# Optimization experiments

Measured on AMD Instinct MI355X. Metric: run time of the kernel, lower is better.

Reference implementation:

```python
import jax, jax.numpy as jnp
import numpy as np

EPS = 1e-8
LAMBDA_SOFTMAX = 9.0   # opt.lambda_softmax (SCAN t2i default)
ITERATION_STEP = 2     # opt.iteration_step
LEAKY_SLOPE = 0.1      # clipped_l2norm leaky relu slope


def l2norm(x, axis):
    norm = jnp.sqrt(jnp.sum(x * x, axis=axis, keepdims=True)) + EPS
    return x / norm


def cosine_sim(a, b, axis):
    w12 = jnp.sum(a * b, axis=axis)
    w1 = jnp.linalg.norm(a, axis=axis)
    w2 = jnp.linalg.norm(b, axis=axis)
    return w12 / jnp.clip(w1 * w2, EPS)


def func_attention_t2i(query, context):
    """query: [C, I, T, D] caption words per (caption, image) pair;
    context: [I, R, D] image regions. Returns weightedContext [C, I, T, D]."""
    # attn = bmm(context, query^T) -> [C, I, R, T]
    attn = jnp.einsum('ird,citd->cirt', context, query)
    # raw_feature_norm == 'clipped_l2norm': LeakyReLU(0.1) then l2norm over queryL
    attn = jax.nn.leaky_relu(attn, LEAKY_SLOPE)
    attn = l2norm(attn, axis=-1)
    # transpose -> [C, I, T, R]; temperature softmax over sourceL (regions)
    attn = jnp.swapaxes(attn, -1, -2)
    attn = jax.nn.softmax(attn * LAMBDA_SOFTMAX, axis=-1)
    # weightedContext = bmm(context^T, attn^T)^T -> [C, I, T, D]
    return jnp.einsum('citr,ird->citd', attn, context)


def setup_inputs() -> dict:
    key = jax.random.key(0)
    ks = jax.random.split(key, 4)
    B, R, T, D = 32, 36, 40, 1024
    # encoder outputs are l2-normalized along the feature dim
    img_emb = l2norm(jax.random.normal(ks[0], (B, R, D), jnp.float32), axis=-1)
    cap_emb = l2norm(jax.random.normal(ks[1], (B, T, D), jnp.float32), axis=-1)
    W_lin = jax.random.normal(ks[2], (2 * D, D), jnp.float32) * 0.02
    b_lin = jnp.zeros((D,), jnp.float32)
    W_gate = jax.random.normal(ks[3], (2 * D, D), jnp.float32) * 0.02
    b_gate = jnp.zeros((D,), jnp.float32)
    return dict(img_emb=img_emb, cap_emb=cap_emb,
                W_lin=W_lin, b_lin=b_lin, W_gate=W_gate, b_gate=b_gate)


def reference(img_emb, cap_emb, W_lin, b_lin, W_gate, b_gate):
    """xattn_score_Text_IMRAM (t2i) with gated memory, summed over iterations.
    Returns similarity score matrix [n_image, n_caption]."""
    C, T, D = cap_emb.shape
    I = img_emb.shape[0]
    # cap_i_expand: each caption repeated across all images
    cap_exp = jnp.broadcast_to(cap_emb[:, None], (C, I, T, D))
    query = cap_exp
    score = jnp.zeros((I, C), cap_emb.dtype)
    for _ in range(ITERATION_STEP):
        wc = func_attention_t2i(query, img_emb)            # [C, I, T, D]
        # cosine similarity per word vs original caption words, mean over words
        row_sim = cosine_sim(cap_exp, wc, axis=-1).mean(-1)  # [C, I]
        score = score + row_sim.T                           # [I, C]
        # gated_memory_t2i
        cat = jnp.concatenate([query, wc], axis=-1)         # [C, I, T, 2D]
        upd = jnp.tanh(cat @ W_lin + b_lin)
        gate = jax.nn.sigmoid(cat @ W_gate + b_gate)
        query = query * gate + upd * (1.0 - gate)
    return score
```

## Files before the change

kernel.cpp:

```cpp
#include <hip/hip_runtime.h>
#include <stdint.h>


typedef unsigned short u16;
typedef __attribute__((ext_vector_type(8))) short bf16x8;
typedef __attribute__((ext_vector_type(4))) float f32x4;

#define MFMA_BF16(a, b, c) __builtin_amdgcn_mfma_f32_16x16x32_bf16((a), (b), (c), 0, 0, 0)

__device__ __forceinline__ float bf2f(u16 u) {
  union { unsigned v; float f; } x; x.v = ((unsigned)u) << 16; return x.f;
}
__device__ __forceinline__ u16 f2bf(float f) {
  union { float f; unsigned v; } x; x.f = f;
  return (u16)((x.v + 0x7fffu + ((x.v >> 16) & 1u)) >> 16);
}
__device__ __forceinline__ float frcp(float x) { return __builtin_amdgcn_rcpf(x); }
__device__ __forceinline__ void gl2lds16(const u16* g, u16* l) {
  __builtin_amdgcn_global_load_lds((const __attribute__((address_space(1))) void*)g,
                                   (__attribute__((address_space(3))) void*)l, 16, 0, 0);
}

__global__ void prep_k(const float* __restrict__ img, const float* __restrict__ cap,
                       const float* __restrict__ Wl, const float* __restrict__ Wg,
                       u16* __restrict__ imgb, u16* __restrict__ capb,
                       u16* __restrict__ WTl, u16* __restrict__ WTg,
                       float* __restrict__ cnorm, u16* __restrict__ cwF0) {
  __shared__ u16 tile[32][33];
  const int b = blockIdx.x, tid = threadIdx.x;
  if (b < 2432) {
    const float* src; u16* dst; int idx;
    if (b < 1152) { src = img; dst = imgb; idx = (b * 256 + tid) * 4; }
    else { src = cap; dst = capb; idx = ((b - 1152) * 256 + tid) * 4; }
    const float4 v = *(const float4*)(src + idx);
    u16 o[4] = {f2bf(v.x), f2bf(v.y), f2bf(v.z), f2bf(v.w)};
    *(uint2*)(dst + idx) = *(const uint2*)o;
  } else if (b < 6528) {
    const int b2 = b - 2432;
    const int bx = b2 & 63, by = (b2 >> 6) & 31, bz = b2 >> 11;
    const float* src = bz ? Wg : Wl;
    u16* dst = bz ? WTg : WTl;
    const int k0 = bx * 32, n0 = by * 32;
    const int tx = tid & 31, ty = tid >> 5;
#pragma unroll
    for (int j = 0; j < 4; ++j)
      tile[ty + 8 * j][tx] = f2bf(src[(size_t)(k0 + ty + 8 * j) * 1024 + n0 + tx]);
    __syncthreads();
#pragma unroll
    for (int j = 0; j < 4; ++j)
      dst[(size_t)(n0 + ty + 8 * j) * 2048 + k0 + tx] = tile[tx][ty + 8 * j];
  } else if (b < 6848) {
    const int wv = tid >> 6, lane = tid & 63;
    const int row = (b - 6528) * 4 + wv;
    const float* p = cap + ((size_t)row << 10) + lane * 16;
    float s = 0.f;
#pragma unroll
    for (int e = 0; e < 16; ++e) { float v = p[e]; s += v * v; }
#pragma unroll
    for (int off = 32; off > 0; off >>= 1) s += __shfl_down(s, off, 64);
    if (lane == 0) cnorm[row] = sqrtf(s);
  } else {
    const int idx = ((b - 6848) * 256 + tid) * 8;
    uint4 z; z.x = z.y = z.z = z.w = 0u;
    *(uint4*)(cwF0 + idx) = z;
  }
}

__global__ __launch_bounds__(256, 2) void gemms_k(
    const u16* __restrict__ capb, const u16* __restrict__ imgb,
    const u16* __restrict__ WTl, const u16* __restrict__ WTg,
    u16* __restrict__ preL, u16* __restrict__ preG,
    u16* __restrict__ cwFL, u16* __restrict__ cwFG,
    const float* __restrict__ bL, const float* __restrict__ bG,
    float* __restrict__ S1, u16* __restrict__ Ghi, u16* __restrict__ Glo) {
  __shared__ __align__(16) char lsU[20480];
  const int bid = blockIdx.x;
  const int tid = threadIdx.x;
  const int wv = tid >> 6, lane = tid & 63;
  const int quad = lane >> 4, l15 = lane & 15;
  const bf16x8 zero8 = {0, 0, 0, 0, 0, 0, 0, 0};

  if (bid < 640) {
    u16* lsA = (u16*)lsU;
    u16* lsB = (u16*)(lsU + 4096);
    const int i = bid & 31, m0 = (bid >> 5) * 64;
    const u16* B = imgb + (size_t)i * 36 * 1024;
    f32x4 acc[3];
#pragma unroll
    for (int b = 0; b < 3; ++b) acc[b] = (f32x4){0.f, 0.f, 0.f, 0.f};
    for (int kt = 0; kt < 32; ++kt) {
      if (kt) __syncthreads();
      const int rr = tid >> 2, j = tid & 3;
      const int js = j ^ ((rr >> 2) & 3);
      gl2lds16(capb + (size_t)(m0 + rr) * 1024 + kt * 32 + js * 8,
               lsA + (size_t)(wv * 64) * 8);
      const int rc = rr < 36 ? rr : 35;
      gl2lds16(B + (size_t)rc * 1024 + kt * 32 + js * 8,
               lsB + (size_t)(wv * 64) * 8);
      __syncthreads();
      const int ra = wv * 16 + l15;
      const bf16x8 a2 = *(const bf16x8*)(lsA + ra * 32 + (quad ^ ((ra >> 2) & 3)) * 8);
      bf16x8 b3[3];
#pragma unroll
      for (int nf = 0; nf < 3; ++nf) {
        const int rb = nf * 16 + l15;
        const bf16x8 bv = *(const bf16x8*)(lsB + rb * 32 + (quad ^ ((rb >> 2) & 3)) * 8);
        b3[nf] = (rb < 36) ? bv : zero8;
      }
#pragma unroll
      for (int nf = 0; nf < 3; ++nf) acc[nf] = MFMA_BF16(a2, b3[nf], acc[nf]);
    }
#pragma unroll
    for (int nf = 0; nf < 3; ++nf)
#pragma unroll
      for (int rg = 0; rg < 4; ++rg) {
        const int m = m0 + wv * 16 + quad * 4 + rg;
        S1[((size_t)i * 1280 + m) * 48 + nf * 16 + l15] = acc[nf][rg];
      }
  } else if (bid < 944) {
    u16* lsA = (u16*)lsU;
    u16* lsBl = (u16*)(lsU + 4096);
    u16* lsBg = (u16*)(lsU + 12288);
    const int b2 = bid - 640;
    const int bm = b2 >> 3, bn = b2 & 7;
    const bool iscap = bm < 20;
    const u16* A = iscap ? capb + (size_t)bm * 64 * 1024
                         : imgb + (size_t)(bm - 20) * 64 * 1024;
    const int kofs = iscap ? 0 : 1024;
    const int wm = (wv & 1) * 32, wn = (wv >> 1) * 64;
    f32x4 accL[2][4], accG[2][4];
#pragma unroll
    for (int a = 0; a < 2; ++a)
#pragma unroll
      for (int b = 0; b < 4; ++b) {
        accL[a][b] = (f32x4){0.f, 0.f, 0.f, 0.f};
        accG[a][b] = (f32x4){0.f, 0.f, 0.f, 0.f};
      }
    for (int kt = 0; kt < 32; ++kt) {
      if (kt) __syncthreads();
      {
        const int row = tid >> 2, c8 = tid & 3;
        const int js = c8 ^ (row & 3);
        gl2lds16(A + (size_t)row * 1024 + kt * 32 + js * 8,
                 lsA + (size_t)(wv * 64) * 8);
      }
#pragma unroll
      for (int s = 0; s < 2; ++s) {
        const int idx = s * 256 + tid;
        const int row = idx >> 2, c8 = idx & 3;
        const int js = c8 ^ (row & 3);
        const size_t bro = (size_t)(bn * 128 + row) * 2048 + kofs + kt * 32 + js * 8;
        gl2lds16(WTl + bro, lsBl + (size_t)(s * 256 + wv * 64) * 8);
        gl2lds16(WTg + bro, lsBg + (size_t)(s * 256 + wv * 64) * 8);
      }
      __syncthreads();
      bf16x8 af[2], bl8[4], bg8[4];
#pragma unroll
      for (int mt = 0; mt < 2; ++mt) {
        const int ra = wm + mt * 16 + l15;
        af[mt] = *(const bf16x8*)(lsA + ra * 32 + (quad ^ (ra & 3)) * 8);
      }
#pragma unroll
      for (int nt = 0; nt < 4; ++nt) {
        const int rb = wn + nt * 16 + l15;
        const int off = rb * 32 + (quad ^ (rb & 3)) * 8;
        bl8[nt] = *(const bf16x8*)(lsBl + off);
        bg8[nt] = *(const bf16x8*)(lsBg + off);
      }
#pragma unroll
      for (int mt = 0; mt < 2; ++mt)
#pragma unroll
        for (int nt = 0; nt < 4; ++nt) {
          accL[mt][nt] = MFMA_BF16(af[mt], bl8[nt], accL[mt][nt]);
          accG[mt][nt] = MFMA_BF16(af[mt], bg8[nt], accG[mt][nt]);
        }
    }
#pragma unroll
    for (int mt = 0; mt < 2; ++mt)
#pragma unroll
      for (int nt = 0; nt < 4; ++nt) {
        const int n = bn * 128 + wn + nt * 16 + l15;
        if (iscap) {
          const float blv = bL[n], bgv = bG[n];
#pragma unroll
          for (int r = 0; r < 4; ++r) {
            const int m = bm * 64 + wm + mt * 16 + quad * 4 + r;
            preL[((size_t)m << 10) + n] = f2bf(accL[mt][nt][r] + blv);
            preG[((size_t)m << 10) + n] = f2bf(accG[mt][nt][r] + bgv);
          }
        } else {
          const int db = n >> 4, l15d = n & 15;
#pragma unroll
          for (int r = 0; r < 4; ++r) {
            const int mi = (bm - 20) * 64 + wm + mt * 16 + quad * 4 + r;
            const int i = (mi * 3641) >> 17;
            const int r36 = mi - i * 36;
            const int ksr = r36 >> 5, qd = (r36 & 31) >> 3, e = r36 & 7;
            const size_t gb =
                ((((size_t)i * 64 + db) * 2 + ksr) * 64 + qd * 16 + l15d) * 8 + e;
            cwFL[gb] = f2bf(accL[mt][nt][r]);
            cwFG[gb] = f2bf(accG[mt][nt][r]);
          }
        }
      }
  } else {
    float* lsS = (float*)lsU;
    const int i = bid - 944;
    for (int k = tid; k < 48 * 52; k += 256) lsS[k] = 0.f;
    const u16* arow[3]; bool avalid[3];
#pragma unroll
    for (int mt = 0; mt < 3; ++mt) {
      const int r = mt * 16 + l15;
      avalid[mt] = r < 36;
      arow[mt] = imgb + ((size_t)(i * 36 + (r < 36 ? r : 35)) << 10);
    }
    f32x4 acc[3][3];
#pragma unroll
    for (int a = 0; a < 3; ++a)
#pragma unroll
      for (int b = 0; b < 3; ++b) acc[a][b] = (f32x4){0.f, 0.f, 0.f, 0.f};
    for (int kk = wv * 8; kk < wv * 8 + 8; ++kk) {
      const int ko = kk * 32 + quad * 8;
      bf16x8 af[3];
#pragma unroll
      for (int mt = 0; mt < 3; ++mt)
        af[mt] = avalid[mt] ? *(const bf16x8*)(arow[mt] + ko) : zero8;
#pragma unroll
      for (int mt = 0; mt < 3; ++mt)
#pragma unroll
        for (int nt = 0; nt < 3; ++nt)
          acc[mt][nt] = MFMA_BF16(af[mt], af[nt], acc[mt][nt]);
    }
    __syncthreads();
#pragma unroll
    for (int mt = 0; mt < 3; ++mt)
#pragma unroll
      for (int nt = 0; nt < 3; ++nt)
#pragma unroll
        for (int rg = 0; rg < 4; ++rg)
          atomicAdd(&lsS[(nt * 16 + l15) * 52 + mt * 16 + quad * 4 + rg],
                    acc[mt][nt][rg]);
    __syncthreads();
    if (wv == 0) {
#pragma unroll
      for (int nt = 0; nt < 3; ++nt) {
        const int rp = nt * 16 + l15;
#pragma unroll
        for (int mt = 0; mt < 3; ++mt) {
          const f32x4 g = *(const f32x4*)&lsS[rp * 52 + mt * 16 + quad * 4];
          u16 hv[4], lv[4];
#pragma unroll
          for (int rg = 0; rg < 4; ++rg) {
            hv[rg] = f2bf(g[rg]);
            lv[rg] = f2bf(g[rg] - bf2f(hv[rg]));
          }
          const size_t gb = ((size_t)i * 48 + rp) * 64 + mt * 16 + quad * 4;
          *(uint2*)(Ghi + gb) = *(const uint2*)hv;
          *(uint2*)(Glo + gb) = *(const uint2*)lv;
        }
      }
    }
    for (int k = tid; k < 48 * 16; k += 256) {
      const size_t gb = ((size_t)i * 48 + (k >> 4)) * 64 + 48 + (k & 15);
      Ghi[gb] = 0; Glo[gb] = 0;
    }
  }
}

__global__ __launch_bounds__(256, 4) void gates2_k(
    const u16* __restrict__ cwFL, const u16* __restrict__ cwFG,
    const u16* __restrict__ P1, const u16* __restrict__ preL,
    const u16* __restrict__ preG, const u16* __restrict__ capb,
    const u16* __restrict__ imgb, float* __restrict__ S2) {
  __shared__ __align__(16) u16 lsPre[3][32 * 128];
  __shared__ __align__(16) float lsS2f[32 * 52];
  const int tid = threadIdx.x;
  const int bid = blockIdx.x;
  const int i = bid & 31, ctt = bid >> 5;
  const int ct0 = ctt * 32;
  const int wv = tid >> 6, lane = tid & 63;
  const int quad = lane >> 4, l15 = lane & 15;

  for (int k = tid; k < 32 * 52; k += 256) lsS2f[k] = 0.f;

  bf16x8 bp[2][2];
#pragma unroll
  for (int nt = 0; nt < 2; ++nt)
#pragma unroll
    for (int ks = 0; ks < 2; ++ks)
      bp[nt][ks] = *(const bf16x8*)(
          P1 + ((size_t)i * 1280 + ct0 + nt * 16 + l15) * 64 + ks * 32 + quad * 8);

  const u16* arow[3]; bool avalid[3];
#pragma unroll
  for (int mt = 0; mt < 3; ++mt) {
    const int r = mt * 16 + l15;
    avalid[mt] = r < 36;
    arow[mt] = imgb + ((size_t)(i * 36 + (r < 36 ? r : 35)) << 10);
  }
  const bf16x8 zero8 = {0, 0, 0, 0, 0, 0, 0, 0};

  f32x4 acc2[3][2];
#pragma unroll
  for (int a = 0; a < 3; ++a)
#pragma unroll
    for (int b = 0; b < 2; ++b) acc2[a][b] = (f32x4){0.f, 0.f, 0.f, 0.f};

#define STAGE(dcx)                                                          \
  {                                                                         \
    _Pragma("unroll")                                                       \
    for (int s = 0; s < 2; ++s) {                                           \
      const int idx = s * 256 + tid;                                        \
      const int rr = idx >> 4, j = idx & 15;                                \
      const int js = j ^ (rr & 7);                                          \
      const size_t src = (size_t)(ct0 + rr) * 1024 + (dcx) * 128 + js * 8;  \
      const size_t dst = (size_t)(s * 256 + wv * 64) * 8;                   \
      gl2lds16(preL + src, lsPre[0] + dst);                                 \
      gl2lds16(preG + src, lsPre[1] + dst);                                 \
      gl2lds16(capb + src, lsPre[2] + dst);                                 \
    }                                                                       \
  }

  STAGE(0);
  for (int dc = 0; dc < 8; ++dc) {
    __syncthreads();

    f32x4 accL[2][2], accG[2][2];
#pragma unroll
    for (int a = 0; a < 2; ++a)
#pragma unroll
      for (int b = 0; b < 2; ++b) {
        accL[a][b] = (f32x4){0.f, 0.f, 0.f, 0.f};
        accG[a][b] = (f32x4){0.f, 0.f, 0.f, 0.f};
      }
#pragma unroll
    for (int mt = 0; mt < 2; ++mt)
#pragma unroll
      for (int ks = 0; ks < 2; ++ks) {
        const int db = dc * 8 + wv * 2 + mt;
        const size_t co = ((((size_t)i * 64 + db) * 2 + ks) * 64 + lane) * 8;
        const bf16x8 al = *(const bf16x8*)(cwFL + co);
        const bf16x8 ag = *(const bf16x8*)(cwFG + co);
#pragma unroll
        for (int nt = 0; nt < 2; ++nt) {
          accL[mt][nt] = MFMA_BF16(al, bp[nt][ks], accL[mt][nt]);
          accG[mt][nt] = MFMA_BF16(ag, bp[nt][ks], accG[mt][nt]);
        }
      }

    uint2 ovv[2][2];
#pragma unroll
    for (int mt = 0; mt < 2; ++mt) {
      const int drel = wv * 32 + mt * 16 + quad * 4;
      const int j = drel >> 3;
#pragma unroll
      for (int nt = 0; nt < 2; ++nt) {
        const int rr = nt * 16 + l15;
        const int off = rr * 128 + (j ^ (rr & 7)) * 8 + (quad & 1) * 4;
        const uint2 plv = *(const uint2*)(lsPre[0] + off);
        const uint2 pgv = *(const uint2*)(lsPre[1] + off);
        const uint2 cfv = *(const uint2*)(lsPre[2] + off);
        const float pl4[4] = {bf2f((u16)(plv.x & 0xffffu)), bf2f((u16)(plv.x >> 16)),
                              bf2f((u16)(plv.y & 0xffffu)), bf2f((u16)(plv.y >> 16))};
        const float pg4[4] = {bf2f((u16)(pgv.x & 0xffffu)), bf2f((u16)(pgv.x >> 16)),
                              bf2f((u16)(pgv.y & 0xffffu)), bf2f((u16)(pgv.y >> 16))};
        const float cf4[4] = {bf2f((u16)(cfv.x & 0xffffu)), bf2f((u16)(cfv.x >> 16)),
                              bf2f((u16)(cfv.y & 0xffffu)), bf2f((u16)(cfv.y >> 16))};
        u16 ov[4];
#pragma unroll
        for (int rg = 0; rg < 4; ++rg) {
          const float aL = accL[mt][nt][rg] + pl4[rg];
          const float aG = accG[mt][nt][rg] + pg4[rg];
          const float g = frcp(1.f + __expf(-aG));
          const float u = 2.f * frcp(1.f + __expf(-2.f * aL)) - 1.f;
          ov[rg] = f2bf(cf4[rg] * g + u * (1.f - g));
        }
        ovv[mt][nt] = *(const uint2*)ov;
      }
    }
    __syncthreads();
    if (dc < 7) STAGE(dc + 1);

#pragma unroll
    for (int nt = 0; nt < 2; ++nt) {
      unsigned w[4];
#pragma unroll
      for (int j2 = 0; j2 < 4; ++j2) {
        const int srcl = ((quad & 1) * 2 + (j2 >> 1)) * 16 + l15;
        const unsigned a0 =
            __shfl((j2 & 1) ? ovv[0][nt].y : ovv[0][nt].x, srcl, 64);
        const unsigned a1 =
            __shfl((j2 & 1) ? ovv[1][nt].y : ovv[1][nt].x, srcl, 64);
        w[j2] = (quad >= 2) ? a1 : a0;
      }
      union { unsigned u[4]; bf16x8 v; } bq;
      bq.u[0] = w[0]; bq.u[1] = w[1]; bq.u[2] = w[2]; bq.u[3] = w[3];
      const int dg = dc * 128 + wv * 32 + quad * 8;
#pragma unroll
      for (int mt = 0; mt < 3; ++mt) {
        const bf16x8 af = avalid[mt] ? *(const bf16x8*)(arow[mt] + dg) : zero8;
        acc2[mt][nt] = MFMA_BF16(af, bq.v, acc2[mt][nt]);
      }
    }
  }
#undef STAGE
#pragma unroll
  for (int mt = 0; mt < 3; ++mt)
#pragma unroll
    for (int nt = 0; nt < 2; ++nt)
#pragma unroll
      for (int rg = 0; rg < 4; ++rg)
        atomicAdd(&lsS2f[(nt * 16 + l15) * 52 + mt * 16 + quad * 4 + rg],
                  acc2[mt][nt][rg]);
  __syncthreads();
  for (int idx = tid; idx < 384; idx += 256) {
    const int ct = idx / 12, rq = idx % 12;
    *(f32x4*)(S2 + ((size_t)i * 1280 + ct0 + ct) * 48 + rq * 4) =
        *(const f32x4*)&lsS2f[ct * 52 + rq * 4];
  }
}

template <int PASS2>
__global__ __launch_bounds__(256, 2) void score_k(
    const float* __restrict__ Ssm, const float* __restrict__ S1,
    const u16* __restrict__ Ghi, const u16* __restrict__ Glo,
    const float* __restrict__ cnorm, u16* __restrict__ P1,
    float* __restrict__ sim1, float* __restrict__ score) {
  __shared__ __align__(16) u16 lsP[4][48 * 72];
  const int tid = threadIdx.x;
  const int wv = tid >> 6, lane = tid & 63;
  const int quad = lane >> 4, l15 = lane & 15;
  const int pair = blockIdx.x * 4 + wv;
  const int c = pair >> 5, i = pair & 31;
  u16* lsPw = lsP[wv];
  for (int k = lane; k < 1728; k += 64) ((unsigned*)lsPw)[k] = 0u;

  float sS[3][3][4], s1f[3][3][4];
  const float* Sb = Ssm + ((size_t)i * 1280 + c * 40) * 48;
  const float* S1b = S1 + ((size_t)i * 1280 + c * 40) * 48;
#pragma unroll
  for (int nt = 0; nt < 3; ++nt) {
    const int t = nt * 16 + l15;
    const int tr = t < 40 ? t : 39;
#pragma unroll
    for (int mt = 0; mt < 3; ++mt) {
      f32x4 v = *(const f32x4*)(Sb + (size_t)tr * 48 + mt * 16 + quad * 4);
      if (t >= 40) v = (f32x4){0.f, 0.f, 0.f, 0.f};
#pragma unroll
      for (int rg = 0; rg < 4; ++rg) sS[mt][nt][rg] = v[rg];
      if (PASS2) {
        const f32x4 w = *(const f32x4*)(S1b + (size_t)tr * 48 + mt * 16 + quad * 4);
#pragma unroll
        for (int rg = 0; rg < 4; ++rg) s1f[mt][nt][rg] = w[rg];
      } else {
#pragma unroll
        for (int rg = 0; rg < 4; ++rg) s1f[mt][nt][rg] = v[rg];
      }
    }
  }

  float rn[3][4];
#pragma unroll
  for (int mt = 0; mt < 3; ++mt)
#pragma unroll
    for (int rg = 0; rg < 4; ++rg) {
      float s2 = 0.f;
#pragma unroll
      for (int nt = 0; nt < 3; ++nt) {
        float v = sS[mt][nt][rg]; v = v > 0.f ? v : 0.1f * v; s2 += v * v;
      }
      s2 += __shfl_xor(s2, 1, 64); s2 += __shfl_xor(s2, 2, 64);
      s2 += __shfl_xor(s2, 4, 64); s2 += __shfl_xor(s2, 8, 64);
      rn[mt][rg] = sqrtf(s2) + 1e-8f;
    }
  float mx[3] = {-3.0e38f, -3.0e38f, -3.0e38f};
#pragma unroll
  for (int mt = 0; mt < 3; ++mt)
#pragma unroll
    for (int nt = 0; nt < 3; ++nt)
#pragma unroll
      for (int rg = 0; rg < 4; ++rg) {
        const int r = mt * 16 + quad * 4 + rg;
        float v = sS[mt][nt][rg]; v = v > 0.f ? v : 0.1f * v;
        float zz = 9.f * v / rn[mt][rg];
        zz = (r < 36) ? zz : -3.0e38f;
        sS[mt][nt][rg] = zz;
        mx[nt] = fmaxf(mx[nt], zz);
      }
#pragma unroll
  for (int nt = 0; nt < 3; ++nt) {
    mx[nt] = fmaxf(mx[nt], __shfl_xor(mx[nt], 16, 64));
    mx[nt] = fmaxf(mx[nt], __shfl_xor(mx[nt], 32, 64));
  }
  float ss[3] = {0.f, 0.f, 0.f};
#pragma unroll
  for (int mt = 0; mt < 3; ++mt)
#pragma unroll
    for (int nt = 0; nt < 3; ++nt)
#pragma unroll
      for (int rg = 0; rg < 4; ++rg) {
        const float e = __expf(sS[mt][nt][rg] - mx[nt]);
        sS[mt][nt][rg] = e; ss[nt] += e;
      }
#pragma unroll
  for (int nt = 0; nt < 3; ++nt) {
    ss[nt] += __shfl_xor(ss[nt], 16, 64);
    ss[nt] += __shfl_xor(ss[nt], 32, 64);
    ss[nt] = 1.f / ss[nt];
  }
#pragma unroll
  for (int nt = 0; nt < 3; ++nt) {
    const int t = nt * 16 + l15;
#pragma unroll
    for (int mt = 0; mt < 3; ++mt) {
#pragma unroll
      for (int rg = 0; rg < 4; ++rg) sS[mt][nt][rg] *= ss[nt];
      if (t < 40) {
        u16 pv[4];
#pragma unroll
        for (int rg = 0; rg < 4; ++rg) pv[rg] = f2bf(sS[mt][nt][rg]);
        *(uint2*)(lsPw + t * 72 + mt * 16 + quad * 4) = *(const uint2*)pv;
      }
    }
  }

  float pnv[3] = {0.f, 0.f, 0.f};
#pragma unroll
  for (int nt = 0; nt < 3; ++nt)
#pragma unroll
    for (int mt = 0; mt < 3; ++mt)
#pragma unroll
      for (int rg = 0; rg < 4; ++rg) pnv[nt] += sS[mt][nt][rg] * s1f[mt][nt][rg];

  if (!PASS2) {
    for (int idx = lane; idx < 320; idx += 64) {
      const int t = idx >> 3, j = idx & 7;
      *(uint4*)(P1 + ((size_t)i * 1280 + c * 40 + t) * 64 + j * 8) =
          *(const uint4*)(lsPw + t * 72 + j * 8);
    }
  }

  bf16x8 afA[3][2];
#pragma unroll
  for (int mtT = 0; mtT < 3; ++mtT)
#pragma unroll
    for (int ks = 0; ks < 2; ++ks)
      afA[mtT][ks] =
          *(const bf16x8*)(lsPw + (mtT * 16 + l15) * 72 + ks * 32 + quad * 8);
  f32x4 gp[3][3];
#pragma unroll
  for (int a = 0; a < 3; ++a)
#pragma unroll
    for (int b = 0; b < 3; ++b) gp[a][b] = (f32x4){0.f, 0.f, 0.f, 0.f};
#pragma unroll
  for (int ks = 0; ks < 2; ++ks)
#pragma unroll
    for (int mtG = 0; mtG < 3; ++mtG) {
      const size_t gb = ((size_t)i * 48 + mtG * 16 + l15) * 64 + ks * 32 + quad * 8;
      const bf16x8 gh = *(const bf16x8*)(Ghi + gb);
      const bf16x8 gl = *(const bf16x8*)(Glo + gb);
#pragma unroll
      for (int mtT = 0; mtT < 3; ++mtT) {
        gp[mtG][mtT] = MFMA_BF16(gh, afA[mtT][ks], gp[mtG][mtT]);
        gp[mtG][mtT] = MFMA_BF16(gl, afA[mtT][ks], gp[mtG][mtT]);
      }
    }
  float pwv[3] = {0.f, 0.f, 0.f};
#pragma unroll
  for (int nt = 0; nt < 3; ++nt)
#pragma unroll
    for (int mt = 0; mt < 3; ++mt)
#pragma unroll
      for (int rg = 0; rg < 4; ++rg)
        pwv[nt] += sS[mt][nt][rg] * gp[mt][nt][rg];
#pragma unroll
  for (int nt = 0; nt < 3; ++nt) {
    pnv[nt] += __shfl_xor(pnv[nt], 16, 64); pnv[nt] += __shfl_xor(pnv[nt], 32, 64);
    pwv[nt] += __shfl_xor(pwv[nt], 16, 64); pwv[nt] += __shfl_xor(pwv[nt], 32, 64);
  }
  float tot = 0.f;
#pragma unroll
  for (int nt = 0; nt < 3; ++nt) {
    const int t = nt * 16 + l15;
    if (t < 40) {
      const float w2 = sqrtf(fmaxf(pwv[nt], 0.f));
      tot += pnv[nt] / fmaxf(cnorm[c * 40 + t] * w2, 1e-8f);
    }
  }
  tot += __shfl_xor(tot, 1, 64); tot += __shfl_xor(tot, 2, 64);
  tot += __shfl_xor(tot, 4, 64); tot += __shfl_xor(tot, 8, 64);
  if (lane == 0) {
    const float s = tot * (1.f / 40.f);
    if (PASS2) score[i * 32 + c] = sim1[pair] + s;
    else sim1[pair] = s;
  }
}

extern "C" void kernel_launch(void* const* d_in, const int* in_sizes, int n_in,
                              void* d_out, int out_size, void* d_ws, size_t ws_size,
                              hipStream_t stream) {
  const float* img = (const float*)d_in[0];
  const float* cap = (const float*)d_in[1];
  const float* Wl  = (const float*)d_in[2];
  const float* bl  = (const float*)d_in[3];
  const float* Wg  = (const float*)d_in[4];
  const float* bg  = (const float*)d_in[5];
  float* out = (float*)d_out;

  char* ws = (char*)d_ws;
  float* cnrm = (float*)ws;               ws += 5120;
  float* sim1 = (float*)ws;               ws += 4096;
  u16*   WTl  = (u16*)ws;                 ws += (size_t)1024 * 2048 * 2;
  u16*   WTg  = (u16*)ws;                 ws += (size_t)1024 * 2048 * 2;
  u16*   preL = (u16*)ws;                 ws += (size_t)1280 * 1024 * 2;
  u16*   preG = (u16*)ws;                 ws += (size_t)1280 * 1024 * 2;
  u16*   capb = (u16*)ws;                 ws += (size_t)1280 * 1024 * 2;
  u16*   imgb = (u16*)ws;                 ws += (size_t)1152 * 1024 * 2;
  u16*   Ghi  = (u16*)ws;                 ws += (size_t)32 * 48 * 64 * 2;
  u16*   Glo  = (u16*)ws;                 ws += (size_t)32 * 48 * 64 * 2;
  u16*   cwFL = (u16*)ws;                 ws += (size_t)32 * 64 * 2 * 64 * 8 * 2;
  u16*   cwFG = (u16*)ws;                 ws += (size_t)32 * 64 * 2 * 64 * 8 * 2;
  float* S1   = (float*)ws;               ws += (size_t)32 * 1280 * 48 * 4;
  float* S2   = (float*)ws;               ws += (size_t)32 * 1280 * 48 * 4;
  u16*   P1   = (u16*)ws;                 ws += (size_t)32 * 1280 * 64 * 2;

  prep_k<<<8896, 256, 0, stream>>>(img, cap, Wl, Wg, imgb, capb, WTl, WTg,
                                   cnrm, cwFL);
  gemms_k<<<976, 256, 0, stream>>>(capb, imgb, WTl, WTg, preL, preG,
                                   cwFL, cwFG, bl, bg, S1, Ghi, Glo);
  score_k<0><<<256, 256, 0, stream>>>(S1, S1, Ghi, Glo, cnrm, P1, sim1, out);
  gates2_k<<<1280, 256, 0, stream>>>(cwFL, cwFG, P1, preL, preG, capb, imgb, S2);
  score_k<1><<<256, 256, 0, stream>>>(S2, S1, Ghi, Glo, cnrm, P1, sim1, out);
}
```

Baseline: 228.8 us.

## Store gate pre-activations and caption in MFMA fragment order, drop LDS staging

The producers (prep_k and gemms_k) now write caption bf16 and the L/G gate pre-activations in a fragment-ordered layout matching the per-lane access pattern of gates2_k. gates2_k then loads them directly from global memory with coalesced 8-byte reads instead of staging 128-column tiles through LDS with async loads and two barriers per chunk. This removes LDS traffic, barriers and LDS footprint, which may allow higher occupancy. The cost is an extra caption copy, scattered 2-byte stores in the gemms epilogue, and loss of the software prefetch overlap, since the 32 blocks per caption tile re-read the data from L2.

```diff
diff --git a/kernel.cpp b/kernel.cpp
--- a/kernel.cpp
+++ b/kernel.cpp
@@ -21,20 +21,34 @@
                                    (__attribute__((address_space(3))) void*)l, 16, 0, 0);
 }
 
+__device__ __forceinline__ size_t fragIdx(int ct, int d) {
+  const int tile = ct >> 5, nt = (ct >> 4) & 1, l15 = ct & 15;
+  const int dc = d >> 7, wvd = (d >> 5) & 3, mt = (d >> 4) & 1;
+  const int quad = (d >> 2) & 3, rg = d & 3;
+  const int lane = quad * 16 + l15;
+  return ((((((size_t)tile * 8 + dc) * 4 + wvd) * 2 + mt) * 2 + nt) * 64 + lane) * 4 + rg;
+}
+
 __global__ void prep_k(const float* __restrict__ img, const float* __restrict__ cap,
                        const float* __restrict__ Wl, const float* __restrict__ Wg,
                        u16* __restrict__ imgb, u16* __restrict__ capb,
+                       u16* __restrict__ capP,
                        u16* __restrict__ WTl, u16* __restrict__ WTg,
                        float* __restrict__ cnorm, u16* __restrict__ cwF0) {
   __shared__ u16 tile[32][33];
   const int b = blockIdx.x, tid = threadIdx.x;
-  if (b < 2432) {
-    const float* src; u16* dst; int idx;
-    if (b < 1152) { src = img; dst = imgb; idx = (b * 256 + tid) * 4; }
-    else { src = cap; dst = capb; idx = ((b - 1152) * 256 + tid) * 4; }
-    const float4 v = *(const float4*)(src + idx);
+  if (b < 1152) {
+    const int idx = (b * 256 + tid) * 4;
+    const float4 v = *(const float4*)(img + idx);
     u16 o[4] = {f2bf(v.x), f2bf(v.y), f2bf(v.z), f2bf(v.w)};
-    *(uint2*)(dst + idx) = *(const uint2*)o;
+    *(uint2*)(imgb + idx) = *(const uint2*)o;
+  } else if (b < 2432) {
+    const int idx = ((b - 1152) * 256 + tid) * 4;
+    const float4 v = *(const float4*)(cap + idx);
+    u16 o[4] = {f2bf(v.x), f2bf(v.y), f2bf(v.z), f2bf(v.w)};
+    *(uint2*)(capb + idx) = *(const uint2*)o;
+    const int ct = idx >> 10, d0 = idx & 1023;
+    *(uint2*)(capP + fragIdx(ct, d0)) = *(const uint2*)o;
   } else if (b < 6528) {
     const int b2 = b - 2432;
     const int bx = b2 & 63, by = (b2 >> 6) & 31, bz = b2 >> 11;
@@ -69,7 +83,7 @@
 __global__ __launch_bounds__(256, 2) void gemms_k(
     const u16* __restrict__ capb, const u16* __restrict__ imgb,
     const u16* __restrict__ WTl, const u16* __restrict__ WTg,
-    u16* __restrict__ preL, u16* __restrict__ preG,
+    u16* __restrict__ prePL, u16* __restrict__ prePG,
     u16* __restrict__ cwFL, u16* __restrict__ cwFG,
     const float* __restrict__ bL, const float* __restrict__ bG,
     float* __restrict__ S1, u16* __restrict__ Ghi, u16* __restrict__ Glo) {
@@ -185,8 +199,9 @@
 #pragma unroll
           for (int r = 0; r < 4; ++r) {
             const int m = bm * 64 + wm + mt * 16 + quad * 4 + r;
-            preL[((size_t)m << 10) + n] = f2bf(accL[mt][nt][r] + blv);
-            preG[((size_t)m << 10) + n] = f2bf(accG[mt][nt][r] + bgv);
+            const size_t fi = fragIdx(m, n);
+            prePL[fi] = f2bf(accL[mt][nt][r] + blv);
+            prePG[fi] = f2bf(accG[mt][nt][r] + bgv);
           }
         } else {
           const int db = n >> 4, l15d = n & 15;
@@ -269,10 +284,9 @@
 
 __global__ __launch_bounds__(256, 4) void gates2_k(
     const u16* __restrict__ cwFL, const u16* __restrict__ cwFG,
-    const u16* __restrict__ P1, const u16* __restrict__ preL,
-    const u16* __restrict__ preG, const u16* __restrict__ capb,
+    const u16* __restrict__ P1, const u16* __restrict__ prePL,
+    const u16* __restrict__ prePG, const u16* __restrict__ capP,
     const u16* __restrict__ imgb, float* __restrict__ S2) {
-  __shared__ __align__(16) u16 lsPre[3][32 * 128];
   __shared__ __align__(16) float lsS2f[32 * 52];
   const int tid = threadIdx.x;
   const int bid = blockIdx.x;
@@ -282,6 +296,7 @@
   const int quad = lane >> 4, l15 = lane & 15;
 
   for (int k = tid; k < 32 * 52; k += 256) lsS2f[k] = 0.f;
+  __syncthreads();
 
   bf16x8 bp[2][2];
 #pragma unroll
@@ -306,25 +321,7 @@
 #pragma unroll
     for (int b = 0; b < 2; ++b) acc2[a][b] = (f32x4){0.f, 0.f, 0.f, 0.f};
 
-#define STAGE(dcx)                                                          \
-  {                                                                         \
-    _Pragma("unroll")                                                       \
-    for (int s = 0; s < 2; ++s) {                                           \
-      const int idx = s * 256 + tid;                                        \
-      const int rr = idx >> 4, j = idx & 15;                                \
-      const int js = j ^ (rr & 7);                                          \
-      const size_t src = (size_t)(ct0 + rr) * 1024 + (dcx) * 128 + js * 8;  \
-      const size_t dst = (size_t)(s * 256 + wv * 64) * 8;                   \
-      gl2lds16(preL + src, lsPre[0] + dst);                                 \
-      gl2lds16(preG + src, lsPre[1] + dst);                                 \
-      gl2lds16(capb + src, lsPre[2] + dst);                                 \
-    }                                                                       \
-  }
-
-  STAGE(0);
   for (int dc = 0; dc < 8; ++dc) {
-    __syncthreads();
-
     f32x4 accL[2][2], accG[2][2];
 #pragma unroll
     for (int a = 0; a < 2; ++a)
@@ -348,18 +345,16 @@
         }
       }
 
+    const size_t fb = (((size_t)ctt * 8 + dc) * 4 + wv) * 2;
     uint2 ovv[2][2];
 #pragma unroll
     for (int mt = 0; mt < 2; ++mt) {
-      const int drel = wv * 32 + mt * 16 + quad * 4;
-      const int j = drel >> 3;
 #pragma unroll
       for (int nt = 0; nt < 2; ++nt) {
-        const int rr = nt * 16 + l15;
-        const int off = rr * 128 + (j ^ (rr & 7)) * 8 + (quad & 1) * 4;
-        const uint2 plv = *(const uint2*)(lsPre[0] + off);
-        const uint2 pgv = *(const uint2*)(lsPre[1] + off);
-        const uint2 cfv = *(const uint2*)(lsPre[2] + off);
+        const size_t fo = (((fb + mt) * 2 + nt) * 64 + lane) * 4;
+        const uint2 plv = *(const uint2*)(prePL + fo);
+        const uint2 pgv = *(const uint2*)(prePG + fo);
+        const uint2 cfv = *(const uint2*)(capP + fo);
         const float pl4[4] = {bf2f((u16)(plv.x & 0xffffu)), bf2f((u16)(plv.x >> 16)),
                               bf2f((u16)(plv.y & 0xffffu)), bf2f((u16)(plv.y >> 16))};
         const float pg4[4] = {bf2f((u16)(pgv.x & 0xffffu)), bf2f((u16)(pgv.x >> 16)),
@@ -378,8 +373,6 @@
         ovv[mt][nt] = *(const uint2*)ov;
       }
     }
-    __syncthreads();
-    if (dc < 7) STAGE(dc + 1);
 
 #pragma unroll
     for (int nt = 0; nt < 2; ++nt) {
@@ -403,7 +396,6 @@
       }
     }
   }
-#undef STAGE
 #pragma unroll
   for (int mt = 0; mt < 3; ++mt)
 #pragma unroll
@@ -612,9 +604,10 @@
   float* sim1 = (float*)ws;               ws += 4096;
   u16*   WTl  = (u16*)ws;                 ws += (size_t)1024 * 2048 * 2;
   u16*   WTg  = (u16*)ws;                 ws += (size_t)1024 * 2048 * 2;
-  u16*   preL = (u16*)ws;                 ws += (size_t)1280 * 1024 * 2;
-  u16*   preG = (u16*)ws;                 ws += (size_t)1280 * 1024 * 2;
+  u16*   prePL= (u16*)ws;                 ws += (size_t)1280 * 1024 * 2;
+  u16*   prePG= (u16*)ws;                 ws += (size_t)1280 * 1024 * 2;
   u16*   capb = (u16*)ws;                 ws += (size_t)1280 * 1024 * 2;
+  u16*   capP = (u16*)ws;                 ws += (size_t)1280 * 1024 * 2;
   u16*   imgb = (u16*)ws;                 ws += (size_t)1152 * 1024 * 2;
   u16*   Ghi  = (u16*)ws;                 ws += (size_t)32 * 48 * 64 * 2;
   u16*   Glo  = (u16*)ws;                 ws += (size_t)32 * 48 * 64 * 2;
@@ -624,11 +617,12 @@
   float* S2   = (float*)ws;               ws += (size_t)32 * 1280 * 48 * 4;
   u16*   P1   = (u16*)ws;                 ws += (size_t)32 * 1280 * 64 * 2;
 
-  prep_k<<<8896, 256, 0, stream>>>(img, cap, Wl, Wg, imgb, capb, WTl, WTg,
-                                   cnrm, cwFL);
-  gemms_k<<<976, 256, 0, stream>>>(capb, imgb, WTl, WTg, preL, preG,
+  prep_k<<<8896, 256, 0, stream>>>(img, cap, Wl, Wg, imgb, capb, capP,
+                                   WTl, WTg, cnrm, cwFL);
+  gemms_k<<<976, 256, 0, stream>>>(capb, imgb, WTl, WTg, prePL, prePG,
                                    cwFL, cwFG, bl, bg, S1, Ghi, Glo);
   score_k<0><<<256, 256, 0, stream>>>(S1, S1, Ghi, Glo, cnrm, P1, sim1, out);
-  gates2_k<<<1280, 256, 0, stream>>>(cwFL, cwFG, P1, preL, preG, capb, imgb, S2);
+  gates2_k<<<1280, 256, 0, stream>>>(cwFL, cwFG, P1, prePL, prePG, capP,
+                                     imgb, S2);
   score_k<1><<<256, 256, 0, stream>>>(S2, S1, Ghi, Glo, cnrm, P1, sim1, out);
 }
```

Measured after the change: 236.7 us. 3.4% more time.
